# Performance work log

Hardware: AMD Instinct MI355X
Metric: run time of the kernel (lower is better)

## Reference

```python
import jax, jax.numpy as jnp
import numpy as np

B, IN_C, OUT_C, NUM, DIM = 4096, 512, 512, 16, 128

def _unif(k, shape, fan_in):
    b = 1.0 / np.sqrt(fan_in)
    return jax.random.uniform(k, shape, jnp.float32, -b, b)

def setup_inputs() -> dict:
    key = jax.random.key(0)
    ks = jax.random.split(key, 9)
    inp = jax.random.normal(ks[0], (B, IN_C), jnp.float32)
    Wpre = _unif(ks[1], (DIM, IN_C), IN_C)        # nn.Linear weight (out, in)
    bpre = _unif(ks[2], (DIM,), IN_C)
    W = _unif(ks[3], (NUM, NUM, DIM, DIM), DIM)    # W[i,j] = link[i][j].weight (out=e, in=d)
    bl = _unif(ks[4], (NUM, NUM, DIM), DIM)        # link biases
    life = jax.random.uniform(ks[5], (NUM, NUM), jnp.float32) + 0.5  # rand(1)+0.5
    Wpost = _unif(ks[6], (OUT_C, DIM), DIM)
    bpost = _unif(ks[7], (OUT_C,), DIM)
    return {"inp": inp, "Wpre": Wpre, "bpre": bpre, "W": W, "b": bl,
            "life": life, "Wpost": Wpost, "bpost": bpost, "steps": 10}

def reference(inp, Wpre, bpre, W, b, life, Wpost, bpost, steps):
    num = life.shape[0]
    x = inp @ Wpre.T + bpre                         # [B, dim]
    gate = jnp.where(life > 0, life, 0.0)           # life>0 branch with scalar gain
    Wg = gate[:, :, None, None] * W                 # [num, num, dim, dim]
    bias = jnp.einsum('ij,ijd->jd', gate, b)        # per-step constant bias sum over i
    m0 = jnp.zeros((num,) + x.shape, x.dtype).at[0].set(x)  # matrix[0] = inp
    def step(m, _):
        # new[j] = sum_i gate[i,j] * (m[i] @ W[i,j].T + b[i,j])
        new = jnp.einsum('ibd,ijed->jbe', m, Wg) + bias[:, None, :]
        return new, None
    mT, _ = jax.lax.scan(step, m0, None, length=steps)
    return mT[num - 1] @ Wpost.T + bpost            # [B, out_c]
```

## Files before the change

kernel.cpp:

```cpp
#include <hip/hip_runtime.h>


typedef __bf16 bf16x8 __attribute__((ext_vector_type(8)));
typedef float f32x4 __attribute__((ext_vector_type(4)));
typedef __attribute__((address_space(3))) unsigned int lds_u32;
typedef const __attribute__((address_space(1))) unsigned int glb_u32;

__device__ __forceinline__ unsigned short f2bf(float x) {
  unsigned int u = __float_as_uint(x);
  u += 0x7FFFu + ((u >> 16) & 1u);
  return (unsigned short)(u >> 16);
}
__device__ __forceinline__ float bf2f(unsigned short s) {
  return __uint_as_float(((unsigned int)s) << 16);
}
__device__ __forceinline__ bf16x8 ldg8(const unsigned short* p) {
  return __builtin_bit_cast(bf16x8, *(const uint4*)p);
}
__device__ __forceinline__ f32x4 mfma16(bf16x8 a, bf16x8 b, f32x4 c) {
  return __builtin_amdgcn_mfma_f32_16x16x32_bf16(a, b, c, 0, 0, 0);
}

#define ND 2048
#define MT 144
#define KS 4
#define CKS 16

__global__ __launch_bounds__(256) void build_all(
    const float* __restrict__ W, const float* __restrict__ life,
    const float* __restrict__ bl, const float* __restrict__ inp,
    unsigned short* __restrict__ Ahi, unsigned short* __restrict__ Alo,
    unsigned short* __restrict__ AThi, unsigned short* __restrict__ ATlo,
    unsigned short* __restrict__ Qhi, unsigned short* __restrict__ Qlo,
    unsigned short* __restrict__ Rhi, unsigned short* __restrict__ Rlo,
    float* __restrict__ beta,
    unsigned short* __restrict__ Ihi, unsigned short* __restrict__ Ilo) {
  __shared__ unsigned short Th[32][36], Tl[32][36];
  const int tid = blockIdx.x * 256 + threadIdx.x;
  const int NT = gridDim.x * 256;
  const int t = threadIdx.x;

  {
    const int r = t >> 3;
    const int c4 = (t & 7) * 4;
    for (int tt = blockIdx.x; tt < 4096; tt += gridDim.x) {
      int nt = tt & 63, kt = tt >> 6;
      int j = nt >> 2, e0 = (nt & 3) * 32;
      int i = kt >> 2, d0 = (kt & 3) * 32;
      float gval = life[i * 16 + j];
      float gate = gval > 0.f ? gval : 0.f;
      const float* src = W + ((size_t)(i * 16 + j) * 16384 + (e0 + r) * 128 + d0 + c4);
      float4 v = *(const float4*)src;
      float vals[4] = {v.x, v.y, v.z, v.w};
      union { unsigned short u[4]; uint2 d2; } oh, ol;
#pragma unroll
      for (int x = 0; x < 4; ++x) {
        float s = gate * vals[x];
        oh.u[x] = f2bf(s);
        ol.u[x] = f2bf(s - bf2f(oh.u[x]));
      }
      size_t aidx = (size_t)(j * 128 + e0 + r) * ND + i * 128 + d0 + c4;
      *(uint2*)(Ahi + aidx) = oh.d2;
      *(uint2*)(Alo + aidx) = ol.d2;
      __syncthreads();
#pragma unroll
      for (int x = 0; x < 4; ++x) { Th[r][c4 + x] = oh.u[x]; Tl[r][c4 + x] = ol.u[x]; }
      __syncthreads();
      union { unsigned short u[4]; uint2 d2; } th, tl;
#pragma unroll
      for (int x = 0; x < 4; ++x) { th.u[x] = Th[c4 + x][r]; tl.u[x] = Tl[c4 + x][r]; }
      size_t tidx = (size_t)(i * 128 + d0 + r) * ND + j * 128 + e0 + c4;
      *(uint2*)(AThi + tidx) = th.d2;
      *(uint2*)(ATlo + tidx) = tl.d2;
    }
  }

  for (int item = tid; item < MT * ND; item += NT) {
    int m = item >> 11, n = item & 2047;
    int j = n >> 7, e = n & 127;
    unsigned short hh = 0, ll = 0;
    if (m < 128) {
      float gval = life[j];
      float gate = gval > 0.f ? gval : 0.f;
      float v = gate * W[j * 16384 + e * 128 + m];
      hh = f2bf(v); ll = f2bf(v - bf2f(hh));
    } else if (m == 128) {
      float s = 0.f;
#pragma unroll
      for (int i = 0; i < 16; ++i) {
        float gval = life[i * 16 + j];
        float gate = gval > 0.f ? gval : 0.f;
        s += gate * bl[(i * 16 + j) * 128 + e];
      }
      beta[n] = s;
      hh = f2bf(s); ll = f2bf(s - bf2f(hh));
    }
    Qhi[item] = hh;
    Qlo[item] = ll;
  }

  for (int item = tid; item < MT * ND; item += NT) {
    int m = item >> 11, n = item & 2047;
    int i = n >> 7, d = n & 127;
    unsigned short hh = 0, ll = 0;
    if (m < 128) {
      float gval = life[i * 16 + 15];
      float gate = gval > 0.f ? gval : 0.f;
      float v = gate * W[(size_t)(i * 16 + 15) * 16384 + m * 128 + d];
      hh = f2bf(v); ll = f2bf(v - bf2f(hh));
    }
    Rhi[item] = hh;
    Rlo[item] = ll;
  }

  for (int item = tid; item < (4096 * 512) / 8; item += NT) {
    int base = item * 8;
    float4 x = *(const float4*)(inp + base), y = *(const float4*)(inp + base + 4);
    float vals[8] = {x.x, x.y, x.z, x.w, y.x, y.y, y.z, y.w};
    union { unsigned short u[8]; uint4 v; } ph, pl;
#pragma unroll
    for (int q = 0; q < 8; ++q) {
      unsigned short h = f2bf(vals[q]);
      ph.u[q] = h;
      pl.u[q] = f2bf(vals[q] - bf2f(h));
    }
    *(uint4*)(Ihi + base) = ph.v;
    *(uint4*)(Ilo + base) = pl.v;
  }
}

__global__ __launch_bounds__(192, 2) void step_pair(
    const unsigned short* __restrict__ Ahi, const unsigned short* __restrict__ Alo,
    const unsigned short* __restrict__ AThi, const unsigned short* __restrict__ ATlo,
    const unsigned short* __restrict__ Qqhi, const unsigned short* __restrict__ Qqlo,
    const unsigned short* __restrict__ Qrhi, const unsigned short* __restrict__ Qrlo,
    float* __restrict__ Pq, float* __restrict__ Pr) {
  __shared__ __align__(16) unsigned short AS[2][64][256];
  const int t = threadIdx.x;
  const int g = t >> 6, lane = t & 63;
  const int r16 = lane & 15, q = lane >> 4;
  const int kc = blockIdx.x;
  const int nb = blockIdx.y;
  const int chain = blockIdx.z;
  const unsigned short* Bh = chain ? AThi : Ahi;
  const unsigned short* Bl = chain ? ATlo : Alo;
  const unsigned short* Qh = chain ? Qrhi : Qqhi;
  const unsigned short* Ql = chain ? Qrlo : Qqlo;
  float* P = chain ? Pr : Pq;
  const int kbase = kc * 512;
  const int n0 = nb * 32;

  for (int ch = g; ch < 64; ch += 3) {
    int half = ch >> 5, c2 = ch & 31;
    int s = c2 * 64 + lane;
    int row = s >> 5;
    int c16 = (s & 31) ^ (row & 7);
    const unsigned short* src =
        (row < 32 ? Bh + (size_t)(n0 + row) * ND
                  : Bl + (size_t)(n0 + row - 32) * ND) + kbase + half * 256 + c16 * 8;
    __builtin_amdgcn_global_load_lds((glb_u32*)src,
                                     (lds_u32*)(&AS[0][0][0] + ch * 512), 16, 0, 0);
  }

  const int m0 = g * 48 + r16;
  const unsigned short* pA0h = Qh + (size_t)m0 * ND + kbase + q * 8;
  const unsigned short* pA0l = Ql + (size_t)m0 * ND + kbase + q * 8;

  bf16x8 qa[2][6];
#pragma unroll
  for (int f = 0; f < 3; ++f) {
    qa[0][2 * f]     = ldg8(pA0h + f * 16 * ND);
    qa[0][2 * f + 1] = ldg8(pA0l + f * 16 * ND);
  }
  __syncthreads();

  const uint4* ASv = (const uint4*)&AS[0][0][0];

  f32x4 acc[3][2];
#pragma unroll
  for (int mt = 0; mt < 3; ++mt)
#pragma unroll
    for (int nt = 0; nt < 2; ++nt) acc[mt][nt] = (f32x4){0.f, 0.f, 0.f, 0.f};

#pragma unroll
  for (int it = 0; it < 16; ++it) {
    const int cur = it & 1, nxt = cur ^ 1;
    if (it < 15) {
      const int ko = (it + 1) * 32;
#pragma unroll
      for (int f = 0; f < 3; ++f) {
        qa[nxt][2 * f]     = ldg8(pA0h + f * 16 * ND + ko);
        qa[nxt][2 * f + 1] = ldg8(pA0l + f * 16 * ND + ko);
      }
    }
    const int hbase = (it >> 3) * 2048;
    const int it8 = it & 7;
    const int cx = (it8 * 4 + q) ^ (r16 & 7);
    bf16x8 b0h = __builtin_bit_cast(bf16x8, ASv[hbase + r16 * 32 + cx]);
    bf16x8 b1h = __builtin_bit_cast(bf16x8, ASv[hbase + (16 + r16) * 32 + cx]);
    bf16x8 b0l = __builtin_bit_cast(bf16x8, ASv[hbase + (32 + r16) * 32 + cx]);
    bf16x8 b1l = __builtin_bit_cast(bf16x8, ASv[hbase + (48 + r16) * 32 + cx]);

    acc[0][0] = mfma16(qa[cur][0], b0h, acc[0][0]);
    acc[0][0] = mfma16(qa[cur][1], b0h, acc[0][0]);
    acc[0][0] = mfma16(qa[cur][0], b0l, acc[0][0]);
    acc[1][0] = mfma16(qa[cur][2], b0h, acc[1][0]);
    acc[1][0] = mfma16(qa[cur][3], b0h, acc[1][0]);
    acc[1][0] = mfma16(qa[cur][2], b0l, acc[1][0]);
    acc[2][0] = mfma16(qa[cur][4], b0h, acc[2][0]);
    acc[2][0] = mfma16(qa[cur][5], b0h, acc[2][0]);
    acc[2][0] = mfma16(qa[cur][4], b0l, acc[2][0]);
    acc[0][1] = mfma16(qa[cur][0], b1h, acc[0][1]);
    acc[0][1] = mfma16(qa[cur][1], b1h, acc[0][1]);
    acc[0][1] = mfma16(qa[cur][0], b1l, acc[0][1]);
    acc[1][1] = mfma16(qa[cur][2], b1h, acc[1][1]);
    acc[1][1] = mfma16(qa[cur][3], b1h, acc[1][1]);
    acc[1][1] = mfma16(qa[cur][2], b1l, acc[1][1]);
    acc[2][1] = mfma16(qa[cur][4], b1h, acc[2][1]);
    acc[2][1] = mfma16(qa[cur][5], b1h, acc[2][1]);
    acc[2][1] = mfma16(qa[cur][4], b1l, acc[2][1]);
  }

  float* Pk = P + kc * (MT * ND);
#pragma unroll
  for (int mt = 0; mt < 3; ++mt)
#pragma unroll
    for (int nt = 0; nt < 2; ++nt) {
      int mbase = g * 48 + mt * 16 + q * 4;
      int n = n0 + nt * 16 + r16;
#pragma unroll
      for (int r = 0; r < 4; ++r)
        Pk[(mbase + r) * ND + n] = acc[mt][nt][r];
    }
}

__global__ __launch_bounds__(256) void reduce_pair(
    const float* __restrict__ Pq, const float* __restrict__ Pr,
    const float* __restrict__ beta,
    unsigned short* __restrict__ Oqh, unsigned short* __restrict__ Oql,
    unsigned short* __restrict__ Orh, unsigned short* __restrict__ Orl) {
  int bid = blockIdx.x;
  int chain = bid >= 288;
  int t = (bid - (chain ? 288 : 0)) * 256 + threadIdx.x;
  const float* P = chain ? Pr : Pq;
  unsigned short* Oh = chain ? Orh : Oqh;
  unsigned short* Ol = chain ? Orl : Oql;
  int m = t >> 9;
  int n = (t & 511) * 4;
  int idx = m * ND + n;
  const int stride = MT * ND;
  float v0 = 0.f, v1 = 0.f, v2 = 0.f, v3 = 0.f;
#pragma unroll
  for (int c = 0; c < KS; ++c) {
    float4 s = *(const float4*)(P + c * stride + idx);
    v0 += s.x; v1 += s.y; v2 += s.z; v3 += s.w;
  }
  if (!chain && m == 128) {
    float4 b4 = *(const float4*)(beta + n);
    v0 += b4.x; v1 += b4.y; v2 += b4.z; v3 += b4.w;
  }
  union { unsigned short u[4]; uint2 d; } h, l;
  float vv[4] = {v0, v1, v2, v3};
#pragma unroll
  for (int i = 0; i < 4; ++i) {
    unsigned short hh = f2bf(vv[i]);
    h.u[i] = hh;
    l.u[i] = f2bf(vv[i] - bf2f(hh));
  }
  *(uint2*)(Oh + idx) = h.d;
  *(uint2*)(Ol + idx) = l.d;
}

__global__ __launch_bounds__(192, 2) void contract_S(
    const unsigned short* __restrict__ R5h, const unsigned short* __restrict__ R5l,
    const unsigned short* __restrict__ Q5h, const unsigned short* __restrict__ Q5l,
    float* __restrict__ CP) {
  __shared__ __align__(16) unsigned short AS[64][128];
  const int t = threadIdx.x;
  const int g = t >> 6, lane = t & 63;
  const int r16 = lane & 15, q = lane >> 4;
  const int kc = blockIdx.x;
  const int nb = blockIdx.y;
  const int kbase = kc * 128;
  const int n0 = nb * 32;

  for (int ch = g; ch < 16; ch += 3) {
    int s = ch * 64 + lane;
    int row = s >> 4;
    int c16 = (s & 15) ^ (row & 7);
    const unsigned short* src =
        (row < 32 ? R5h + (size_t)(n0 + row) * ND
                  : R5l + (size_t)(n0 + row - 32) * ND) + kbase + c16 * 8;
    __builtin_amdgcn_global_load_lds((glb_u32*)src,
                                     (lds_u32*)(&AS[0][0] + ch * 512), 16, 0, 0);
  }

  const int m0 = g * 48 + r16;
  const unsigned short* pA0h = Q5h + (size_t)m0 * ND + kbase + q * 8;
  const unsigned short* pA0l = Q5l + (size_t)m0 * ND + kbase + q * 8;

  bf16x8 qa[2][6];
#pragma unroll
  for (int f = 0; f < 3; ++f) {
    qa[0][2 * f]     = ldg8(pA0h + f * 16 * ND);
    qa[0][2 * f + 1] = ldg8(pA0l + f * 16 * ND);
  }
  __syncthreads();

  const uint4* ASv = (const uint4*)&AS[0][0];

  f32x4 acc[3][2];
#pragma unroll
  for (int mt = 0; mt < 3; ++mt)
#pragma unroll
    for (int nt = 0; nt < 2; ++nt) acc[mt][nt] = (f32x4){0.f, 0.f, 0.f, 0.f};

#pragma unroll
  for (int it = 0; it < 4; ++it) {
    const int cur = it & 1, nxt = cur ^ 1;
    if (it < 3) {
      const int ko = (it + 1) * 32;
#pragma unroll
      for (int f = 0; f < 3; ++f) {
        qa[nxt][2 * f]     = ldg8(pA0h + f * 16 * ND + ko);
        qa[nxt][2 * f + 1] = ldg8(pA0l + f * 16 * ND + ko);
      }
    }
    const int cx = (it * 4 + q) ^ (r16 & 7);
    bf16x8 b0h = __builtin_bit_cast(bf16x8, ASv[r16 * 16 + cx]);
    bf16x8 b1h = __builtin_bit_cast(bf16x8, ASv[(16 + r16) * 16 + cx]);
    bf16x8 b0l = __builtin_bit_cast(bf16x8, ASv[(32 + r16) * 16 + cx]);
    bf16x8 b1l = __builtin_bit_cast(bf16x8, ASv[(48 + r16) * 16 + cx]);

    acc[0][0] = mfma16(qa[cur][0], b0h, acc[0][0]);
    acc[0][0] = mfma16(qa[cur][1], b0h, acc[0][0]);
    acc[0][0] = mfma16(qa[cur][0], b0l, acc[0][0]);
    acc[1][0] = mfma16(qa[cur][2], b0h, acc[1][0]);
    acc[1][0] = mfma16(qa[cur][3], b0h, acc[1][0]);
    acc[1][0] = mfma16(qa[cur][2], b0l, acc[1][0]);
    acc[2][0] = mfma16(qa[cur][4], b0h, acc[2][0]);
    acc[2][0] = mfma16(qa[cur][5], b0h, acc[2][0]);
    acc[2][0] = mfma16(qa[cur][4], b0l, acc[2][0]);
    acc[0][1] = mfma16(qa[cur][0], b1h, acc[0][1]);
    acc[0][1] = mfma16(qa[cur][1], b1h, acc[0][1]);
    acc[0][1] = mfma16(qa[cur][0], b1l, acc[0][1]);
    acc[1][1] = mfma16(qa[cur][2], b1h, acc[1][1]);
    acc[1][1] = mfma16(qa[cur][3], b1h, acc[1][1]);
    acc[1][1] = mfma16(qa[cur][2], b1l, acc[1][1]);
    acc[2][1] = mfma16(qa[cur][4], b1h, acc[2][1]);
    acc[2][1] = mfma16(qa[cur][5], b1h, acc[2][1]);
    acc[2][1] = mfma16(qa[cur][4], b1l, acc[2][1]);
  }

  float* Pk = CP + kc * (MT * 128);
#pragma unroll
  for (int mt = 0; mt < 3; ++mt)
#pragma unroll
    for (int nt = 0; nt < 2; ++nt) {
      int mbase = g * 48 + mt * 16 + q * 4;
      int n = n0 + nt * 16 + r16;
#pragma unroll
      for (int r = 0; r < 4; ++r)
        Pk[(mbase + r) * 128 + n] = acc[mt][nt][r];
    }
}

__global__ __launch_bounds__(256) void extract_Sc(
    const float* __restrict__ CP,
    const unsigned short* __restrict__ Q5h, const unsigned short* __restrict__ Q5l,
    float* __restrict__ St, float* __restrict__ gv) {
  int t = blockIdx.x * 256 + threadIdx.x;
  const int PSTR = MT * 128;
  if (t < 16384) {
    int d = t >> 7, e = t & 127;
    float v = 0.f;
#pragma unroll
    for (int c = 0; c < CKS; ++c) v += CP[c * PSTR + d * 128 + e];
    St[t] = v;
  } else if (t < 16512) {
    int e = t - 16384;
    float v = bf2f(Q5h[128 * ND + 1920 + e]) + bf2f(Q5l[128 * ND + 1920 + e]);
#pragma unroll
    for (int c = 0; c < CKS; ++c) v += CP[c * PSTR + 128 * 128 + e];
    gv[e] = v;
  }
}

__global__ __launch_bounds__(256) void tail_T1g(
    const float* __restrict__ St, const float* __restrict__ Wpre,
    const float* __restrict__ bpre, float* __restrict__ T1,
    float* __restrict__ gv) {
  int t = blockIdx.x * 256 + threadIdx.x;
  if (t < 65536) {
    int e = t >> 9, ic = t & 511;
    float s = 0.f;
    for (int d = 0; d < 128; ++d) s += St[d * 128 + e] * Wpre[d * 512 + ic];
    T1[t] = s;
  } else if (t < 65664) {
    int e = t - 65536;
    float s = gv[e];
    for (int d = 0; d < 128; ++d) s += St[d * 128 + e] * bpre[d];
    gv[e] = s;
  }
}

__global__ __launch_bounds__(256) void tail_Weff(
    const float* __restrict__ Wpost, const float* __restrict__ T1,
    const float* __restrict__ gv, const float* __restrict__ bpost,
    unsigned short* __restrict__ Whi, unsigned short* __restrict__ Wlo,
    float* __restrict__ beff) {
  int t = blockIdx.x * 256 + threadIdx.x;
  if (t < 262144) {
    int o = t >> 9, ic = t & 511;
    float s = 0.f;
    for (int e = 0; e < 128; ++e) s += Wpost[o * 128 + e] * T1[e * 512 + ic];
    unsigned short h = f2bf(s);
    Whi[t] = h;
    Wlo[t] = f2bf(s - bf2f(h));
  } else if (t < 262656) {
    int o = t - 262144;
    float s = bpost[o];
    for (int e = 0; e < 128; ++e) s += Wpost[o * 128 + e] * gv[e];
    beff[o] = s;
  }
}

__global__ __launch_bounds__(256) void final_gemm(
    const unsigned short* __restrict__ Ihi, const unsigned short* __restrict__ Ilo,
    const unsigned short* __restrict__ Whi, const unsigned short* __restrict__ Wlo,
    const float* __restrict__ beff, float* __restrict__ out) {
  __shared__ __align__(16) unsigned short Is_hi[64][40], Is_lo[64][40];
  __shared__ __align__(16) unsigned short Ws_hi[128][40], Ws_lo[128][40];
  const int t = threadIdx.x;
  const int mb = blockIdx.x, nb = blockIdx.y;
  const int w = t >> 6, lane = t & 63;
  const int r16 = lane & 15, q = lane >> 4;

  f32x4 acc[4][2];
#pragma unroll
  for (int x = 0; x < 4; ++x)
#pragma unroll
    for (int b = 0; b < 2; ++b) acc[x][b] = (f32x4){0.f, 0.f, 0.f, 0.f};

  for (int kc = 0; kc < 16; ++kc) {
    const int k0 = kc * 32;
#pragma unroll
    for (int rpt = 0; rpt < 6; ++rpt) {
      int slot = t + rpt * 256;
      if (slot < 512) {
        int arr = slot >> 8, s = slot & 255;
        int row = s >> 2, off = (s & 3) * 8;
        const unsigned short* src = arr ? Ilo : Ihi;
        unsigned short* dst = arr ? &Is_lo[row][off] : &Is_hi[row][off];
        *(uint4*)dst = *(const uint4*)(src + (mb * 64 + row) * 512 + k0 + off);
      } else {
        int s = slot - 512;
        int arr = s >> 9, s2 = s & 511;
        int row = s2 >> 2, off = (s2 & 3) * 8;
        const unsigned short* src = arr ? Wlo : Whi;
        unsigned short* dst = arr ? &Ws_lo[row][off] : &Ws_hi[row][off];
        *(uint4*)dst = *(const uint4*)(src + (nb * 128 + row) * 512 + k0 + off);
      }
    }
    __syncthreads();

    bf16x8 bh0 = __builtin_bit_cast(bf16x8, *(const uint4*)&Ws_hi[w * 32 + r16][q * 8]);
    bf16x8 bl0 = __builtin_bit_cast(bf16x8, *(const uint4*)&Ws_lo[w * 32 + r16][q * 8]);
    bf16x8 bh1 = __builtin_bit_cast(bf16x8, *(const uint4*)&Ws_hi[w * 32 + 16 + r16][q * 8]);
    bf16x8 bl1 = __builtin_bit_cast(bf16x8, *(const uint4*)&Ws_lo[w * 32 + 16 + r16][q * 8]);
#pragma unroll
    for (int mt = 0; mt < 4; ++mt) {
      bf16x8 ah = __builtin_bit_cast(bf16x8, *(const uint4*)&Is_hi[mt * 16 + r16][q * 8]);
      bf16x8 al = __builtin_bit_cast(bf16x8, *(const uint4*)&Is_lo[mt * 16 + r16][q * 8]);
      acc[mt][0] = mfma16(ah, bh0, acc[mt][0]);
      acc[mt][0] = mfma16(al, bh0, acc[mt][0]);
      acc[mt][0] = mfma16(ah, bl0, acc[mt][0]);
      acc[mt][1] = mfma16(ah, bh1, acc[mt][1]);
      acc[mt][1] = mfma16(al, bh1, acc[mt][1]);
      acc[mt][1] = mfma16(ah, bl1, acc[mt][1]);
    }
    __syncthreads();
  }

#pragma unroll
  for (int mt = 0; mt < 4; ++mt)
#pragma unroll
    for (int nt = 0; nt < 2; ++nt) {
      int n = nb * 128 + w * 32 + nt * 16 + r16;
      float bv = beff[n];
#pragma unroll
      for (int r = 0; r < 4; ++r) {
        int m = mb * 64 + mt * 16 + q * 4 + r;
        out[m * 512 + n] = acc[mt][nt][r] + bv;
      }
    }
}

extern "C" void kernel_launch(void* const* d_in, const int* in_sizes, int n_in,
                              void* d_out, int out_size, void* d_ws, size_t ws_size,
                              hipStream_t stream) {
  const float* inp   = (const float*)d_in[0];
  const float* Wpre  = (const float*)d_in[1];
  const float* bpre  = (const float*)d_in[2];
  const float* W     = (const float*)d_in[3];
  const float* bl    = (const float*)d_in[4];
  const float* life  = (const float*)d_in[5];
  const float* Wpost = (const float*)d_in[6];
  const float* bpost = (const float*)d_in[7];
  float* out = (float*)d_out;

  char* p = (char*)d_ws;
  auto alloc = [&](size_t bytes) {
    char* r = p;
    p += (bytes + 255) & ~(size_t)255;
    return r;
  };
  unsigned short* Ahi  = (unsigned short*)alloc((size_t)ND * ND * 2);
  unsigned short* Alo  = (unsigned short*)alloc((size_t)ND * ND * 2);
  unsigned short* AThi = (unsigned short*)alloc((size_t)ND * ND * 2);
  unsigned short* ATlo = (unsigned short*)alloc((size_t)ND * ND * 2);
  unsigned short* QqAh = (unsigned short*)alloc((size_t)MT * ND * 2);
  unsigned short* QqAl = (unsigned short*)alloc((size_t)MT * ND * 2);
  unsigned short* QqBh = (unsigned short*)alloc((size_t)MT * ND * 2);
  unsigned short* QqBl = (unsigned short*)alloc((size_t)MT * ND * 2);
  unsigned short* QrAh = (unsigned short*)alloc((size_t)MT * ND * 2);
  unsigned short* QrAl = (unsigned short*)alloc((size_t)MT * ND * 2);
  unsigned short* QrBh = (unsigned short*)alloc((size_t)MT * ND * 2);
  unsigned short* QrBl = (unsigned short*)alloc((size_t)MT * ND * 2);
  float* beta = (float*)alloc(ND * 4);
  float* Pq   = (float*)alloc((size_t)KS * MT * ND * 4);
  float* Pr   = (float*)alloc((size_t)KS * MT * ND * 4);
  float* CP   = (float*)alloc((size_t)CKS * MT * 128 * 4);
  float* St   = (float*)alloc(128 * 128 * 4);
  float* gv   = (float*)alloc(128 * 4);
  float* T1   = (float*)alloc(128 * 512 * 4);
  float* beff = (float*)alloc(512 * 4);
  unsigned short* Whi = (unsigned short*)alloc(512 * 512 * 2);
  unsigned short* Wlo = (unsigned short*)alloc(512 * 512 * 2);
  unsigned short* Ihi = (unsigned short*)alloc((size_t)4096 * 512 * 2);
  unsigned short* Ilo = (unsigned short*)alloc((size_t)4096 * 512 * 2);

  build_all<<<1024, 256, 0, stream>>>(W, life, bl, inp, Ahi, Alo, AThi, ATlo,
                                      QqAh, QqAl, QrAh, QrAl, beta, Ihi, Ilo);

  const unsigned short *qqh = QqAh, *qql = QqAl, *qrh = QrAh, *qrl = QrAl;
  unsigned short *oqh = QqBh, *oql = QqBl, *orh = QrBh, *orl = QrBl;
  for (int s = 0; s < 4; ++s) {
    step_pair<<<dim3(KS, 64, 2), 192, 0, stream>>>(
        Ahi, Alo, AThi, ATlo, qqh, qql, qrh, qrl, Pq, Pr);
    reduce_pair<<<576, 256, 0, stream>>>(Pq, Pr, beta, oqh, oql, orh, orl);
    const unsigned short* t1 = qqh; qqh = oqh; oqh = (unsigned short*)t1;
    const unsigned short* t2 = qql; qql = oql; oql = (unsigned short*)t2;
    const unsigned short* t3 = qrh; qrh = orh; orh = (unsigned short*)t3;
    const unsigned short* t4 = qrl; qrl = orl; orl = (unsigned short*)t4;
  }

  contract_S<<<dim3(CKS, 4), 192, 0, stream>>>(qrh, qrl, qqh, qql, CP);
  extract_Sc<<<65, 256, 0, stream>>>(CP, qqh, qql, St, gv);
  tail_T1g<<<257, 256, 0, stream>>>(St, Wpre, bpre, T1, gv);
  tail_Weff<<<1026, 256, 0, stream>>>(Wpost, T1, gv, bpost, Whi, Wlo, beff);
  final_gemm<<<dim3(64, 4), 256, 0, stream>>>(Ihi, Ilo, Whi, Wlo, beff, out);
}
```

Before: 247.3 us.

## Refactor tail into three low-rank GEMMs and atomically reduce contract_S output

Instead of building an effective 512x512 weight with scalar FP32 loops (tail_T1g and tail_Weff), the tail now applies the factors in sequence: X1 = inp·Wpreᵀ (issued before the step loop), X2 = X1·S, out = X2·Wpostᵀ + beff. Each product is a split-bf16 MFMA GEMM. contract_S now accumulates straight into St/gv with atomicAdd, which removes the CP partial buffer and the extract kernel. The aim is to drop the slow naive scalar tail kernels and a launch. The cost is an extra X1/X2 round trip through memory and float atomics, which make the summation order nondeterministic.

```diff
diff --git a/kernel.cpp b/kernel.cpp
--- a/kernel.cpp
+++ b/kernel.cpp
@@ -29,12 +29,16 @@
 __global__ __launch_bounds__(256) void build_all(
     const float* __restrict__ W, const float* __restrict__ life,
     const float* __restrict__ bl, const float* __restrict__ inp,
+    const float* __restrict__ Wpre, const float* __restrict__ Wpost,
     unsigned short* __restrict__ Ahi, unsigned short* __restrict__ Alo,
     unsigned short* __restrict__ AThi, unsigned short* __restrict__ ATlo,
     unsigned short* __restrict__ Qhi, unsigned short* __restrict__ Qlo,
     unsigned short* __restrict__ Rhi, unsigned short* __restrict__ Rlo,
     float* __restrict__ beta,
-    unsigned short* __restrict__ Ihi, unsigned short* __restrict__ Ilo) {
+    unsigned short* __restrict__ Ihi, unsigned short* __restrict__ Ilo,
+    unsigned short* __restrict__ Wph, unsigned short* __restrict__ Wpl,
+    unsigned short* __restrict__ Woh, unsigned short* __restrict__ Wol,
+    float* __restrict__ St, float* __restrict__ gv) {
   __shared__ unsigned short Th[32][36], Tl[32][36];
   const int tid = blockIdx.x * 256 + threadIdx.x;
   const int NT = gridDim.x * 256;
@@ -126,6 +130,30 @@
     }
     *(uint4*)(Ihi + base) = ph.v;
     *(uint4*)(Ilo + base) = pl.v;
+  }
+
+  for (int item = tid; item < 16384; item += NT) {
+    const float* src = (item < 8192) ? Wpre : Wpost;
+    unsigned short* dh = (item < 8192) ? Wph : Woh;
+    unsigned short* dl = (item < 8192) ? Wpl : Wol;
+    int base = (item < 8192 ? item : item - 8192) * 8;
+    float4 x = *(const float4*)(src + base), y = *(const float4*)(src + base + 4);
+    float vals[8] = {x.x, x.y, x.z, x.w, y.x, y.y, y.z, y.w};
+    union { unsigned short u[8]; uint4 v; } ph, pl;
+#pragma unroll
+    for (int q = 0; q < 8; ++q) {
+      unsigned short h = f2bf(vals[q]);
+      ph.u[q] = h;
+      pl.u[q] = f2bf(vals[q] - bf2f(h));
+    }
+    *(uint4*)(dh + base) = ph.v;
+    *(uint4*)(dl + base) = pl.v;
+  }
+
+  for (int item = tid; item < 4128; item += NT) {
+    float4 z = {0.f, 0.f, 0.f, 0.f};
+    if (item < 4096) *(float4*)(St + item * 4) = z;
+    else             *(float4*)(gv + (item - 4096) * 4) = z;
   }
 }
 
@@ -274,7 +302,7 @@
 __global__ __launch_bounds__(192, 2) void contract_S(
     const unsigned short* __restrict__ R5h, const unsigned short* __restrict__ R5l,
     const unsigned short* __restrict__ Q5h, const unsigned short* __restrict__ Q5l,
-    float* __restrict__ CP) {
+    float* __restrict__ St, float* __restrict__ gv) {
   __shared__ __align__(16) unsigned short AS[64][128];
   const int t = threadIdx.x;
   const int g = t >> 6, lane = t & 63;
@@ -352,7 +380,6 @@
     acc[2][1] = mfma16(qa[cur][4], b1l, acc[2][1]);
   }
 
-  float* Pk = CP + kc * (MT * 128);
 #pragma unroll
   for (int mt = 0; mt < 3; ++mt)
 #pragma unroll
@@ -360,79 +387,59 @@
       int mbase = g * 48 + mt * 16 + q * 4;
       int n = n0 + nt * 16 + r16;
 #pragma unroll
-      for (int r = 0; r < 4; ++r)
-        Pk[(mbase + r) * 128 + n] = acc[mt][nt][r];
-    }
-}
-
-__global__ __launch_bounds__(256) void extract_Sc(
-    const float* __restrict__ CP,
+      for (int r = 0; r < 4; ++r) {
+        int m = mbase + r;
+        if (m < 128)       atomicAdd(St + m * 128 + n, acc[mt][nt][r]);
+        else if (m == 128) atomicAdd(gv + n, acc[mt][nt][r]);
+      }
+    }
+}
+
+__global__ __launch_bounds__(256) void tail_small(
+    const float* __restrict__ St, const float* __restrict__ gv,
     const unsigned short* __restrict__ Q5h, const unsigned short* __restrict__ Q5l,
-    float* __restrict__ St, float* __restrict__ gv) {
-  int t = blockIdx.x * 256 + threadIdx.x;
-  const int PSTR = MT * 128;
-  if (t < 16384) {
-    int d = t >> 7, e = t & 127;
-    float v = 0.f;
-#pragma unroll
-    for (int c = 0; c < CKS; ++c) v += CP[c * PSTR + d * 128 + e];
-    St[t] = v;
-  } else if (t < 16512) {
-    int e = t - 16384;
-    float v = bf2f(Q5h[128 * ND + 1920 + e]) + bf2f(Q5l[128 * ND + 1920 + e]);
-#pragma unroll
-    for (int c = 0; c < CKS; ++c) v += CP[c * PSTR + 128 * 128 + e];
-    gv[e] = v;
-  }
-}
-
-__global__ __launch_bounds__(256) void tail_T1g(
-    const float* __restrict__ St, const float* __restrict__ Wpre,
-    const float* __restrict__ bpre, float* __restrict__ T1,
-    float* __restrict__ gv) {
-  int t = blockIdx.x * 256 + threadIdx.x;
-  if (t < 65536) {
-    int e = t >> 9, ic = t & 511;
-    float s = 0.f;
-    for (int d = 0; d < 128; ++d) s += St[d * 128 + e] * Wpre[d * 512 + ic];
-    T1[t] = s;
-  } else if (t < 65664) {
-    int e = t - 65536;
-    float s = gv[e];
-    for (int d = 0; d < 128; ++d) s += St[d * 128 + e] * bpre[d];
-    gv[e] = s;
-  }
-}
-
-__global__ __launch_bounds__(256) void tail_Weff(
-    const float* __restrict__ Wpost, const float* __restrict__ T1,
-    const float* __restrict__ gv, const float* __restrict__ bpost,
-    unsigned short* __restrict__ Whi, unsigned short* __restrict__ Wlo,
+    const float* __restrict__ bpre, const float* __restrict__ Wpost,
+    const float* __restrict__ bpost,
+    unsigned short* __restrict__ Seh, unsigned short* __restrict__ Sel,
     float* __restrict__ beff) {
-  int t = blockIdx.x * 256 + threadIdx.x;
-  if (t < 262144) {
-    int o = t >> 9, ic = t & 511;
-    float s = 0.f;
-    for (int e = 0; e < 128; ++e) s += Wpost[o * 128 + e] * T1[e * 512 + ic];
-    unsigned short h = f2bf(s);
-    Whi[t] = h;
-    Wlo[t] = f2bf(s - bf2f(h));
-  } else if (t < 262656) {
-    int o = t - 262144;
-    float s = bpost[o];
-    for (int e = 0; e < 128; ++e) s += Wpost[o * 128 + e] * gv[e];
-    beff[o] = s;
-  }
-}
-
-__global__ __launch_bounds__(256) void final_gemm(
+  const int t = threadIdx.x;
+  if (blockIdx.x == 0) {
+    __shared__ float gl[128];
+    if (t < 128) {
+      int idx = 128 * ND + 1920 + t;
+      float s = gv[t] + bf2f(Q5h[idx]) + bf2f(Q5l[idx]);
+      for (int d = 0; d < 128; ++d) s += St[d * 128 + t] * bpre[d];
+      gl[t] = s;
+    }
+    __syncthreads();
+    for (int o = t; o < 512; o += 256) {
+      float s = bpost[o];
+      for (int e = 0; e < 128; ++e) s += Wpost[o * 128 + e] * gl[e];
+      beff[o] = s;
+    }
+  } else {
+    int base = (blockIdx.x - 1) * 1024 + t * 4;
+    int e = base >> 7, d0 = base & 127;
+    union { unsigned short u[4]; uint2 d2; } h, l;
+#pragma unroll
+    for (int i = 0; i < 4; ++i) {
+      float v = St[(d0 + i) * 128 + e];
+      h.u[i] = f2bf(v);
+      l.u[i] = f2bf(v - bf2f(h.u[i]));
+    }
+    *(uint2*)(Seh + base) = h.d2;
+    *(uint2*)(Sel + base) = l.d2;
+  }
+}
+
+__global__ __launch_bounds__(256) void gemm_X1(
     const unsigned short* __restrict__ Ihi, const unsigned short* __restrict__ Ilo,
-    const unsigned short* __restrict__ Whi, const unsigned short* __restrict__ Wlo,
-    const float* __restrict__ beff, float* __restrict__ out) {
+    const unsigned short* __restrict__ Wph, const unsigned short* __restrict__ Wpl,
+    unsigned short* __restrict__ X1h, unsigned short* __restrict__ X1l) {
   __shared__ __align__(16) unsigned short Is_hi[64][40], Is_lo[64][40];
   __shared__ __align__(16) unsigned short Ws_hi[128][40], Ws_lo[128][40];
   const int t = threadIdx.x;
-  const int mb = blockIdx.x, nb = blockIdx.y;
+  const int mb = blockIdx.x;
   const int w = t >> 6, lane = t & 63;
   const int r16 = lane & 15, q = lane >> 4;
 
@@ -457,9 +464,155 @@
         int s = slot - 512;
         int arr = s >> 9, s2 = s & 511;
         int row = s2 >> 2, off = (s2 & 3) * 8;
-        const unsigned short* src = arr ? Wlo : Whi;
+        const unsigned short* src = arr ? Wpl : Wph;
         unsigned short* dst = arr ? &Ws_lo[row][off] : &Ws_hi[row][off];
-        *(uint4*)dst = *(const uint4*)(src + (nb * 128 + row) * 512 + k0 + off);
+        *(uint4*)dst = *(const uint4*)(src + row * 512 + k0 + off);
+      }
+    }
+    __syncthreads();
+
+    bf16x8 bh0 = __builtin_bit_cast(bf16x8, *(const uint4*)&Ws_hi[w * 32 + r16][q * 8]);
+    bf16x8 bl0 = __builtin_bit_cast(bf16x8, *(const uint4*)&Ws_lo[w * 32 + r16][q * 8]);
+    bf16x8 bh1 = __builtin_bit_cast(bf16x8, *(const uint4*)&Ws_hi[w * 32 + 16 + r16][q * 8]);
+    bf16x8 bl1 = __builtin_bit_cast(bf16x8, *(const uint4*)&Ws_lo[w * 32 + 16 + r16][q * 8]);
+#pragma unroll
+    for (int mt = 0; mt < 4; ++mt) {
+      bf16x8 ah = __builtin_bit_cast(bf16x8, *(const uint4*)&Is_hi[mt * 16 + r16][q * 8]);
+      bf16x8 al = __builtin_bit_cast(bf16x8, *(const uint4*)&Is_lo[mt * 16 + r16][q * 8]);
+      acc[mt][0] = mfma16(ah, bh0, acc[mt][0]);
+      acc[mt][0] = mfma16(al, bh0, acc[mt][0]);
+      acc[mt][0] = mfma16(ah, bl0, acc[mt][0]);
+      acc[mt][1] = mfma16(ah, bh1, acc[mt][1]);
+      acc[mt][1] = mfma16(al, bh1, acc[mt][1]);
+      acc[mt][1] = mfma16(ah, bl1, acc[mt][1]);
+    }
+    __syncthreads();
+  }
+
+#pragma unroll
+  for (int mt = 0; mt < 4; ++mt)
+#pragma unroll
+    for (int nt = 0; nt < 2; ++nt) {
+      int n = w * 32 + nt * 16 + r16;
+#pragma unroll
+      for (int r = 0; r < 4; ++r) {
+        int m = mb * 64 + mt * 16 + q * 4 + r;
+        float v = acc[mt][nt][r];
+        unsigned short h = f2bf(v);
+        X1h[m * 128 + n] = h;
+        X1l[m * 128 + n] = f2bf(v - bf2f(h));
+      }
+    }
+}
+
+__global__ __launch_bounds__(256) void gemm_X2(
+    const unsigned short* __restrict__ X1h, const unsigned short* __restrict__ X1l,
+    const unsigned short* __restrict__ Seh, const unsigned short* __restrict__ Sel,
+    unsigned short* __restrict__ X2h, unsigned short* __restrict__ X2l) {
+  __shared__ __align__(16) unsigned short Is_hi[64][40], Is_lo[64][40];
+  __shared__ __align__(16) unsigned short Ws_hi[128][40], Ws_lo[128][40];
+  const int t = threadIdx.x;
+  const int mb = blockIdx.x;
+  const int w = t >> 6, lane = t & 63;
+  const int r16 = lane & 15, q = lane >> 4;
+
+  f32x4 acc[4][2];
+#pragma unroll
+  for (int x = 0; x < 4; ++x)
+#pragma unroll
+    for (int b = 0; b < 2; ++b) acc[x][b] = (f32x4){0.f, 0.f, 0.f, 0.f};
+
+  for (int kc = 0; kc < 4; ++kc) {
+    const int k0 = kc * 32;
+#pragma unroll
+    for (int rpt = 0; rpt < 6; ++rpt) {
+      int slot = t + rpt * 256;
+      if (slot < 512) {
+        int arr = slot >> 8, s = slot & 255;
+        int row = s >> 2, off = (s & 3) * 8;
+        const unsigned short* src = arr ? X1l : X1h;
+        unsigned short* dst = arr ? &Is_lo[row][off] : &Is_hi[row][off];
+        *(uint4*)dst = *(const uint4*)(src + (mb * 64 + row) * 128 + k0 + off);
+      } else {
+        int s = slot - 512;
+        int arr = s >> 9, s2 = s & 511;
+        int row = s2 >> 2, off = (s2 & 3) * 8;
+        const unsigned short* src = arr ? Sel : Seh;
+        unsigned short* dst = arr ? &Ws_lo[row][off] : &Ws_hi[row][off];
+        *(uint4*)dst = *(const uint4*)(src + row * 128 + k0 + off);
+      }
+    }
+    __syncthreads();
+
+    bf16x8 bh0 = __builtin_bit_cast(bf16x8, *(const uint4*)&Ws_hi[w * 32 + r16][q * 8]);
+    bf16x8 bl0 = __builtin_bit_cast(bf16x8, *(const uint4*)&Ws_lo[w * 32 + r16][q * 8]);
+    bf16x8 bh1 = __builtin_bit_cast(bf16x8, *(const uint4*)&Ws_hi[w * 32 + 16 + r16][q * 8]);
+    bf16x8 bl1 = __builtin_bit_cast(bf16x8, *(const uint4*)&Ws_lo[w * 32 + 16 + r16][q * 8]);
+#pragma unroll
+    for (int mt = 0; mt < 4; ++mt) {
+      bf16x8 ah = __builtin_bit_cast(bf16x8, *(const uint4*)&Is_hi[mt * 16 + r16][q * 8]);
+      bf16x8 al = __builtin_bit_cast(bf16x8, *(const uint4*)&Is_lo[mt * 16 + r16][q * 8]);
+      acc[mt][0] = mfma16(ah, bh0, acc[mt][0]);
+      acc[mt][0] = mfma16(al, bh0, acc[mt][0]);
+      acc[mt][0] = mfma16(ah, bl0, acc[mt][0]);
+      acc[mt][1] = mfma16(ah, bh1, acc[mt][1]);
+      acc[mt][1] = mfma16(al, bh1, acc[mt][1]);
+      acc[mt][1] = mfma16(ah, bl1, acc[mt][1]);
+    }
+    __syncthreads();
+  }
+
+#pragma unroll
+  for (int mt = 0; mt < 4; ++mt)
+#pragma unroll
+    for (int nt = 0; nt < 2; ++nt) {
+      int n = w * 32 + nt * 16 + r16;
+#pragma unroll
+      for (int r = 0; r < 4; ++r) {
+        int m = mb * 64 + mt * 16 + q * 4 + r;
+        float v = acc[mt][nt][r];
+        unsigned short h = f2bf(v);
+        X2h[m * 128 + n] = h;
+        X2l[m * 128 + n] = f2bf(v - bf2f(h));
+      }
+    }
+}
+
+__global__ __launch_bounds__(256) void gemm_X3(
+    const unsigned short* __restrict__ X2h, const unsigned short* __restrict__ X2l,
+    const unsigned short* __restrict__ Woh, const unsigned short* __restrict__ Wol,
+    const float* __restrict__ beff, float* __restrict__ out) {
+  __shared__ __align__(16) unsigned short Is_hi[64][40], Is_lo[64][40];
+  __shared__ __align__(16) unsigned short Ws_hi[128][40], Ws_lo[128][40];
+  const int t = threadIdx.x;
+  const int mb = blockIdx.x, nb = blockIdx.y;
+  const int w = t >> 6, lane = t & 63;
+  const int r16 = lane & 15, q = lane >> 4;
+
+  f32x4 acc[4][2];
+#pragma unroll
+  for (int x = 0; x < 4; ++x)
+#pragma unroll
+    for (int b = 0; b < 2; ++b) acc[x][b] = (f32x4){0.f, 0.f, 0.f, 0.f};
+
+  for (int kc = 0; kc < 4; ++kc) {
+    const int k0 = kc * 32;
+#pragma unroll
+    for (int rpt = 0; rpt < 6; ++rpt) {
+      int slot = t + rpt * 256;
+      if (slot < 512) {
+        int arr = slot >> 8, s = slot & 255;
+        int row = s >> 2, off = (s & 3) * 8;
+        const unsigned short* src = arr ? X2l : X2h;
+        unsigned short* dst = arr ? &Is_lo[row][off] : &Is_hi[row][off];
+        *(uint4*)dst = *(const uint4*)(src + (mb * 64 + row) * 128 + k0 + off);
+      } else {
+        int s = slot - 512;
+        int arr = s >> 9, s2 = s & 511;
+        int row = s2 >> 2, off = (s2 & 3) * 8;
+        const unsigned short* src = arr ? Wol : Woh;
+        unsigned short* dst = arr ? &Ws_lo[row][off] : &Ws_hi[row][off];
+        *(uint4*)dst = *(const uint4*)(src + (nb * 128 + row) * 128 + k0 + off);
       }
     }
     __syncthreads();
@@ -530,18 +683,27 @@
   float* beta = (float*)alloc(ND * 4);
   float* Pq   = (float*)alloc((size_t)KS * MT * ND * 4);
   float* Pr   = (float*)alloc((size_t)KS * MT * ND * 4);
-  float* CP   = (float*)alloc((size_t)CKS * MT * 128 * 4);
   float* St   = (float*)alloc(128 * 128 * 4);
   float* gv   = (float*)alloc(128 * 4);
-  float* T1   = (float*)alloc(128 * 512 * 4);
   float* beff = (float*)alloc(512 * 4);
-  unsigned short* Whi = (unsigned short*)alloc(512 * 512 * 2);
-  unsigned short* Wlo = (unsigned short*)alloc(512 * 512 * 2);
   unsigned short* Ihi = (unsigned short*)alloc((size_t)4096 * 512 * 2);
   unsigned short* Ilo = (unsigned short*)alloc((size_t)4096 * 512 * 2);
-
-  build_all<<<1024, 256, 0, stream>>>(W, life, bl, inp, Ahi, Alo, AThi, ATlo,
-                                      QqAh, QqAl, QrAh, QrAl, beta, Ihi, Ilo);
+  unsigned short* Wph = (unsigned short*)alloc(128 * 512 * 2);
+  unsigned short* Wpl = (unsigned short*)alloc(128 * 512 * 2);
+  unsigned short* Woh = (unsigned short*)alloc(512 * 128 * 2);
+  unsigned short* Wol = (unsigned short*)alloc(512 * 128 * 2);
+  unsigned short* Seh = (unsigned short*)alloc(128 * 128 * 2);
+  unsigned short* Sel = (unsigned short*)alloc(128 * 128 * 2);
+  unsigned short* X1h = (unsigned short*)alloc((size_t)4096 * 128 * 2);
+  unsigned short* X1l = (unsigned short*)alloc((size_t)4096 * 128 * 2);
+  unsigned short* X2h = (unsigned short*)alloc((size_t)4096 * 128 * 2);
+  unsigned short* X2l = (unsigned short*)alloc((size_t)4096 * 128 * 2);
+
+  build_all<<<1024, 256, 0, stream>>>(W, life, bl, inp, Wpre, Wpost,
+                                      Ahi, Alo, AThi, ATlo,
+                                      QqAh, QqAl, QrAh, QrAl, beta, Ihi, Ilo,
+                                      Wph, Wpl, Woh, Wol, St, gv);
+  gemm_X1<<<dim3(64, 1), 256, 0, stream>>>(Ihi, Ilo, Wph, Wpl, X1h, X1l);
 
   const unsigned short *qqh = QqAh, *qql = QqAl, *qrh = QrAh, *qrl = QrAl;
   unsigned short *oqh = QqBh, *oql = QqBl, *orh = QrBh, *orl = QrBl;
@@ -555,9 +717,9 @@
     const unsigned short* t4 = qrl; qrl = orl; orl = (unsigned short*)t4;
   }
 
-  contract_S<<<dim3(CKS, 4), 192, 0, stream>>>(qrh, qrl, qqh, qql, CP);
-  extract_Sc<<<65, 256, 0, stream>>>(CP, qqh, qql, St, gv);
-  tail_T1g<<<257, 256, 0, stream>>>(St, Wpre, bpre, T1, gv);
-  tail_Weff<<<1026, 256, 0, stream>>>(Wpost, T1, gv, bpost, Whi, Wlo, beff);
-  final_gemm<<<dim3(64, 4), 256, 0, stream>>>(Ihi, Ilo, Whi, Wlo, beff, out);
-}
+  contract_S<<<dim3(CKS, 4), 192, 0, stream>>>(qrh, qrl, qqh, qql, St, gv);
+  tail_small<<<17, 256, 0, stream>>>(St, gv, qqh, qql, bpre, Wpost, bpost,
+                                     Seh, Sel, beff);
+  gemm_X2<<<dim3(64, 1), 256, 0, stream>>>(X1h, X1l, Seh, Sel, X2h, X2l);
+  gemm_X3<<<dim3(64, 4), 256, 0, stream>>>(X2h, X2l, Woh, Wol, beff, out);
+}
```

After: 247.6 us. About the same (+0.1%).
